# Optimization experiments

Measured on AMD Instinct MI355X. Metric: run time of the kernel, lower is better.

The kernel has to match this reference:

```python
import jax, jax.numpy as jnp
import numpy as np

G, M_PER_GROUP, K, N = 8, 2048, 4096, 4096  # experts, tokens/expert, d_model, expert out dim


def setup_inputs() -> dict:
    key = jax.random.key(0)
    k1, k2, k3, k4 = jax.random.split(key, 4)
    T = G * M_PER_GROUP
    # int8 quantized activations [total_tokens, K] and per-expert weights [G, N, K] ('NT' layout)
    i8_left_tensor = jax.random.randint(k1, (T, K), -127, 128, dtype=jnp.int32).astype(jnp.int8)
    i8_right_tensors = jax.random.randint(k2, (G, N, K), -127, 128, dtype=jnp.int32).astype(jnp.int8)
    # per-token and per-(group, out-channel) dequant scales
    left_scales = jax.random.uniform(k3, (T,), jnp.float32, 0.001, 0.02)
    right_scales = jax.random.uniform(k4, (G, N), jnp.float32, 0.001, 0.02)
    tokens_per_group = jnp.full((G,), M_PER_GROUP, dtype=jnp.int32)
    return {
        "i8_left_tensor": i8_left_tensor,
        "i8_right_tensors": i8_right_tensors,
        "left_scales": left_scales,
        "right_scales": right_scales,
        "tokens_per_group": tokens_per_group,
    }


def reference(i8_left_tensor, i8_right_tensors, left_scales, right_scales, tokens_per_group):
    # moe_w8a8_group_gemm, 'NT': per group g, out_g = (A_g @ B_g^T) * ls_g[:, None] * rs_g[None, :] -> fp16
    g, n, k = i8_right_tensors.shape
    t = i8_left_tensor.shape[0]
    m = t // g  # equal-sized groups (tokens_per_group is constant M_PER_GROUP)
    a = i8_left_tensor.reshape(g, m, k).astype(jnp.float32)   # [G, M, K]
    b = i8_right_tensors.astype(jnp.float32)                  # [G, N, K]
    acc = jnp.einsum('gmk,gnk->gmn', a, b)                    # int8xint8 accum in f32
    ls = left_scales.reshape(g, m, 1)
    rs = right_scales[:, None, :]
    out = (acc * ls * rs).astype(jnp.float16)                 # fused dequant epilogue
    return out.reshape(t, n)
```

## Files before the change

kernel.cpp:

```cpp
#include <hip/hip_runtime.h>

#define GG 8
#define MPG 2048
#define KD 4096
#define ND 4096

using i32x4 = __attribute__((ext_vector_type(4))) int;

__device__ __forceinline__ int pack4(i32x4 v) {
  return (int)((unsigned)(v[0] & 0xff) | ((unsigned)(v[1] & 0xff) << 8) |
               ((unsigned)(v[2] & 0xff) << 16) | ((unsigned)(v[3] & 0xff) << 24));
}

__global__ void conv_kernel(const int* __restrict__ src, char* __restrict__ dst, long nelem) {
  long t = (long)blockIdx.x * blockDim.x + threadIdx.x;
  long stride = (long)gridDim.x * blockDim.x;
  for (long e = t * 16; e < nelem; e += stride * 16) {
    i32x4 x0 = *(const i32x4*)(src + e);
    i32x4 x1 = *(const i32x4*)(src + e + 4);
    i32x4 x2 = *(const i32x4*)(src + e + 8);
    i32x4 x3 = *(const i32x4*)(src + e + 12);
    i32x4 p;
    p[0] = pack4(x0); p[1] = pack4(x1); p[2] = pack4(x2); p[3] = pack4(x3);
    *(i32x4*)(dst + e) = p;
  }
}

__device__ __forceinline__ void gload_lds16(const void* g, void* l) {
  __builtin_amdgcn_global_load_lds(
      (const __attribute__((address_space(1))) unsigned int*)g,
      (__attribute__((address_space(3))) unsigned int*)l, 16, 0, 0);
}

#define CFENCE() asm volatile("" ::: "memory")

constexpr int NT = KD / 128;

__global__ __launch_bounds__(512, 2) void gemm256_i8(
    const char* __restrict__ Aall,
    const char* __restrict__ Ball,
    const float* __restrict__ ls,
    const float* __restrict__ rs,
    float* __restrict__ out,
    int g0, int nwg)
{
  extern __shared__ char lds[];

  const int tid  = threadIdx.x;
  const int lane = tid & 63;
  const int wave = tid >> 6;

  int bid = blockIdx.x;
  int wg  = (bid & 7) * (nwg >> 3) + (bid >> 3);
  const int gl = wg >> 7;
  const int rr_ = wg & 127;
  const int bm = (rr_ >> 4) * 256;
  const int bn = (rr_ & 15) * 256;
  const int g  = g0 + gl;

  const int srow = tid >> 3;
  const int scol = ((tid & 7) << 4) ^ ((srow & 7) << 4);
  const char* Ag = Aall + ((size_t)gl * MPG + bm) * KD;
  const char* Bg = Ball + ((size_t)gl * ND  + bn) * KD;
  const char* pa[4]; const char* pb[4];
#pragma unroll
  for (int i = 0; i < 4; ++i) {
    pa[i] = Ag + (size_t)(i * 64 + srow) * KD + scol;
    pb[i] = Bg + (size_t)(i * 64 + srow) * KD + scol;
  }
  char* wbase = lds + wave * 1024;

  auto stageA = [&](int buf, int kt) {
    const int ko = kt << 7;
    char* d = wbase + buf * 65536;
#pragma unroll
    for (int i = 0; i < 4; ++i) gload_lds16(pa[i] + ko, d + i * 8192);
  };
  auto stageB = [&](int buf, int kt) {
    const int ko = kt << 7;
    char* d = wbase + buf * 65536 + 32768;
#pragma unroll
    for (int i = 0; i < 4; ++i) gload_lds16(pb[i] + ko, d + i * 8192);
  };

  const int wm = wave >> 2;
  const int wn = wave & 3;
  const int r16 = lane & 15;
  const int klane = (lane >> 4) << 4;
  const int sx = (r16 & 7) << 4;
  const char* aBase0 = lds + (size_t)(wm * 128 + r16) * 128;
  const char* bBase0 = lds + 32768 + (size_t)(wn * 64 + r16) * 128;

  i32x4 acc[8][4] = {};

  stageA(0, 0); stageB(0, 0);
  stageA(1, 1); stageB(1, 1);

#pragma unroll 1
  for (int kt = 0; kt < NT; ++kt) {
    const int c = kt & 1;
    const char* pA = aBase0 + c * 65536;
    const char* pB = bBase0 + c * 65536;
    const int kx0 = klane ^ sx;
    const int kx1 = (64 + klane) ^ sx;

    if (kt + 1 < NT) { asm volatile("s_waitcnt vmcnt(8)" ::: "memory"); }
    else             { asm volatile("s_waitcnt vmcnt(0)" ::: "memory"); }
    __builtin_amdgcn_s_barrier();
    CFENCE();

    i32x4 bf0[4], bf1[4], af0[4], af1[4];
#pragma unroll
    for (int n = 0; n < 4; ++n) bf0[n] = *(const i32x4*)(pB + n * 2048 + kx0);
#pragma unroll
    for (int m = 0; m < 4; ++m) af0[m] = *(const i32x4*)(pA + m * 2048 + kx0);
#pragma unroll
    for (int m = 0; m < 4; ++m) af1[m] = *(const i32x4*)(pA + (4 + m) * 2048 + kx0);
    __builtin_amdgcn_s_setprio(1);
#pragma unroll
    for (int m = 0; m < 4; ++m)
#pragma unroll
      for (int n = 0; n < 4; ++n)
        acc[m][n] = __builtin_amdgcn_mfma_i32_16x16x64_i8(af0[m], bf0[n], acc[m][n], 0, 0, 0);
    __builtin_amdgcn_s_setprio(0);
#pragma unroll
    for (int n = 0; n < 4; ++n) bf1[n] = *(const i32x4*)(pB + n * 2048 + kx1);
#pragma unroll
    for (int m = 0; m < 4; ++m) af0[m] = *(const i32x4*)(pA + m * 2048 + kx1);
    __builtin_amdgcn_s_setprio(1);
#pragma unroll
    for (int m = 0; m < 4; ++m)
#pragma unroll
      for (int n = 0; n < 4; ++n)
        acc[4 + m][n] = __builtin_amdgcn_mfma_i32_16x16x64_i8(af1[m], bf0[n], acc[4 + m][n], 0, 0, 0);
    __builtin_amdgcn_s_setprio(0);
#pragma unroll
    for (int m = 0; m < 4; ++m) af1[m] = *(const i32x4*)(pA + (4 + m) * 2048 + kx1);
    __builtin_amdgcn_s_setprio(1);
#pragma unroll
    for (int m = 0; m < 4; ++m)
#pragma unroll
      for (int n = 0; n < 4; ++n)
        acc[m][n] = __builtin_amdgcn_mfma_i32_16x16x64_i8(af0[m], bf1[n], acc[m][n], 0, 0, 0);
#pragma unroll
    for (int m = 0; m < 4; ++m)
#pragma unroll
      for (int n = 0; n < 4; ++n)
        acc[4 + m][n] = __builtin_amdgcn_mfma_i32_16x16x64_i8(af1[m], bf1[n], acc[4 + m][n], 0, 0, 0);
    __builtin_amdgcn_s_setprio(0);

    asm volatile("s_waitcnt lgkmcnt(0)" ::: "memory");
    __builtin_amdgcn_sched_barrier(0);
    __builtin_amdgcn_s_barrier();
    CFENCE();
    if (kt + 2 < NT) { stageA(c, kt + 2); stageB(c, kt + 2); }
  }

  const size_t orow0 = (size_t)g * MPG + bm + wm * 128 + ((lane >> 4) << 2);
  const int col0 = bn + wn * 64 + r16;
  float rsv[4];
#pragma unroll
  for (int n = 0; n < 4; ++n) rsv[n] = rs[(size_t)g * ND + col0 + n * 16];
#pragma unroll
  for (int m = 0; m < 8; ++m) {
#pragma unroll
    for (int q = 0; q < 4; ++q) {
      size_t row = orow0 + m * 16 + q;
      float lsv = ls[row];
#pragma unroll
      for (int n = 0; n < 4; ++n)
        out[row * ND + col0 + n * 16] = (float)acc[m][n][q] * lsv * rsv[n];
    }
  }
}

constexpr int BM = 128, BN = 128, BK = 64;

template<bool DIRECT>
__global__ __launch_bounds__(256) void gemm_i8(
    const void* __restrict__ Aptr, const void* __restrict__ Bptr,
    const float* __restrict__ ls, const float* __restrict__ rs,
    float* __restrict__ out, int g0)
{
  __shared__ char lA[BM * BK];
  __shared__ char lB[BN * BK];

  const int gl = blockIdx.z;
  const int g = g0 + gl;
  const int bm = blockIdx.y * BM;
  const int bn = blockIdx.x * BN;
  const int tid = threadIdx.x;
  const int lane = tid & 63;
  const int wave = tid >> 6;
  const int wr = (wave >> 1) * 64;
  const int wc = (wave & 1) * 64;
  const int r16 = lane & 15;
  const int kb = (lane >> 4) * 16;

  i32x4 acc[4][4] = {};

  if constexpr (!DIRECT) {
    const char* Ag = (const char*)Aptr + ((size_t)gl * MPG + bm) * KD;
    const char* Bg = (const char*)Bptr + ((size_t)gl * ND + bn) * KD;
    const int srow = tid >> 2;
    const int skoff = (tid & 3) * 16;
    const char* pa0 = Ag + (size_t)srow * KD + skoff;
    const char* pa1 = Ag + (size_t)(srow + 64) * KD + skoff;
    const char* pb0 = Bg + (size_t)srow * KD + skoff;
    const char* pb1 = Bg + (size_t)(srow + 64) * KD + skoff;
    char* la0 = lA + wave * 1024;
    char* la1 = lA + 4096 + wave * 1024;
    char* lb0 = lB + wave * 1024;
    char* lb1 = lB + 4096 + wave * 1024;

    for (int k0 = 0; k0 < KD; k0 += BK) {
      gload_lds16(pa0 + k0, la0);
      gload_lds16(pa1 + k0, la1);
      gload_lds16(pb0 + k0, lb0);
      gload_lds16(pb1 + k0, lb1);
      __syncthreads();
      i32x4 af[4], bf[4];
#pragma unroll
      for (int m = 0; m < 4; ++m) af[m] = *(const i32x4*)(lA + (wr + m * 16 + r16) * BK + kb);
#pragma unroll
      for (int n = 0; n < 4; ++n) bf[n] = *(const i32x4*)(lB + (wc + n * 16 + r16) * BK + kb);
#pragma unroll
      for (int m = 0; m < 4; ++m)
#pragma unroll
        for (int n = 0; n < 4; ++n)
          acc[m][n] = __builtin_amdgcn_mfma_i32_16x16x64_i8(af[m], bf[n], acc[m][n], 0, 0, 0);
      __syncthreads();
    }
  } else {
    const int* Ag = (const int*)Aptr + ((size_t)gl * MPG + bm) * KD;
    const int* Bg = (const int*)Bptr + ((size_t)gl * ND + bn) * KD;
    const int drow = tid >> 1;
    const int dk = (tid & 1) * 32;

    for (int k0 = 0; k0 < KD; k0 += BK) {
      int pa[8], pb[8];
#pragma unroll
      for (int j = 0; j < 8; ++j) pa[j] = pack4(*(const i32x4*)(Ag + (size_t)drow * KD + k0 + dk + j * 4));
#pragma unroll
      for (int j = 0; j < 8; ++j) pb[j] = pack4(*(const i32x4*)(Bg + (size_t)drow * KD + k0 + dk + j * 4));
      __syncthreads();
      *(i32x4*)(lA + drow * 64 + dk)      = *(i32x4*)(pa);
      *(i32x4*)(lA + drow * 64 + dk + 16) = *(i32x4*)(pa + 4);
      *(i32x4*)(lB + drow * 64 + dk)      = *(i32x4*)(pb);
      *(i32x4*)(lB + drow * 64 + dk + 16) = *(i32x4*)(pb + 4);
      __syncthreads();
      i32x4 af[4], bf[4];
#pragma unroll
      for (int m = 0; m < 4; ++m) af[m] = *(const i32x4*)(lA + (wr + m * 16 + r16) * BK + kb);
#pragma unroll
      for (int n = 0; n < 4; ++n) bf[n] = *(const i32x4*)(lB + (wc + n * 16 + r16) * BK + kb);
#pragma unroll
      for (int m = 0; m < 4; ++m)
#pragma unroll
        for (int n = 0; n < 4; ++n)
          acc[m][n] = __builtin_amdgcn_mfma_i32_16x16x64_i8(af[m], bf[n], acc[m][n], 0, 0, 0);
    }
  }

  const size_t trow0 = (size_t)g * MPG + bm + wr + (lane >> 4) * 4;
  const int col0 = bn + wc + r16;
  float rsv[4];
#pragma unroll
  for (int n = 0; n < 4; ++n) rsv[n] = rs[(size_t)g * ND + col0 + n * 16];
#pragma unroll
  for (int m = 0; m < 4; ++m) {
#pragma unroll
    for (int q = 0; q < 4; ++q) {
      size_t row = trow0 + m * 16 + q;
      float lsv = ls[row];
#pragma unroll
      for (int n = 0; n < 4; ++n)
        out[row * ND + col0 + n * 16] = (float)acc[m][n][q] * lsv * rsv[n];
    }
  }
}

extern "C" void kernel_launch(void* const* d_in, const int* in_sizes, int n_in,
                              void* d_out, int out_size, void* d_ws, size_t ws_size,
                              hipStream_t stream) {
  const int* A32 = (const int*)d_in[0];
  const int* B32 = (const int*)d_in[1];
  const float* ls = (const float*)d_in[2];
  const float* rs = (const float*)d_in[3];
  float* out = (float*)d_out;

  const size_t aE = (size_t)GG * MPG * KD;
  const size_t bE = (size_t)GG * ND * KD;
  const size_t aSlab = (size_t)MPG * KD;
  const size_t bSlab = (size_t)ND * KD;

  const int smem = 131072;
  bool big_lds_ok =
      hipFuncSetAttribute((const void*)gemm256_i8,
                          hipFuncAttributeMaxDynamicSharedMemorySize, smem) == hipSuccess;

  if (d_ws && ws_size >= aE + bE) {
    char* wsA = (char*)d_ws;
    char* wsB = wsA + aE;
    conv_kernel<<<8192, 256, 0, stream>>>(A32, wsA, (long)aE);
    conv_kernel<<<16384, 256, 0, stream>>>(B32, wsB, (long)bE);
    if (big_lds_ok) {
      gemm256_i8<<<1024, 512, smem, stream>>>(wsA, wsB, ls, rs, out, 0, 1024);
    } else {
      dim3 grid(ND / BN, MPG / BM, GG);
      gemm_i8<false><<<grid, dim3(256), 0, stream>>>(wsA, wsB, ls, rs, out, 0);
    }
  } else if (d_ws && ws_size >= aSlab + bSlab) {
    char* wsA = (char*)d_ws;
    char* wsB = wsA + aSlab;
    for (int gidx = 0; gidx < GG; ++gidx) {
      conv_kernel<<<2048, 256, 0, stream>>>(A32 + (size_t)gidx * aSlab, wsA, (long)aSlab);
      conv_kernel<<<4096, 256, 0, stream>>>(B32 + (size_t)gidx * bSlab, wsB, (long)bSlab);
      if (big_lds_ok) {
        gemm256_i8<<<128, 512, smem, stream>>>(wsA, wsB, ls, rs, out, gidx, 128);
      } else {
        dim3 grid(ND / BN, MPG / BM, 1);
        gemm_i8<false><<<grid, dim3(256), 0, stream>>>(wsA, wsB, ls, rs, out, gidx);
      }
    }
  } else {
    dim3 grid(ND / BN, MPG / BM, GG);
    gemm_i8<true><<<grid, dim3(256), 0, stream>>>(A32, B32, ls, rs, out, 0);
  }
}
```

Baseline: 496.6 us.

## Load B fragments directly from global into registers, keep only A in LDS

The B operand no longer goes through LDS. Each wave loads its B fragments straight from global memory into registers, while A keeps a double-buffered LDS path with one barrier per k-step. This halves dynamic LDS to 64 KB, removes the B staging and the second barrier per iteration, and may allow more workgroups per CU. In exchange, global-load latency for B sits directly in front of the MFMAs, the per-lane loads stride across rows and coalesce poorly, and waves that share columns fetch the same B data twice.

Measured after the change: 562.6 us. +13.3%, slower.

```diff
diff --git a/kernel.cpp b/kernel.cpp
--- a/kernel.cpp
+++ b/kernel.cpp
@@ -61,26 +61,16 @@
   const int srow = tid >> 3;
   const int scol = ((tid & 7) << 4) ^ ((srow & 7) << 4);
   const char* Ag = Aall + ((size_t)gl * MPG + bm) * KD;
-  const char* Bg = Ball + ((size_t)gl * ND  + bn) * KD;
-  const char* pa[4]; const char* pb[4];
-#pragma unroll
-  for (int i = 0; i < 4; ++i) {
-    pa[i] = Ag + (size_t)(i * 64 + srow) * KD + scol;
-    pb[i] = Bg + (size_t)(i * 64 + srow) * KD + scol;
-  }
+  const char* pa[4];
+#pragma unroll
+  for (int i = 0; i < 4; ++i) pa[i] = Ag + (size_t)(i * 64 + srow) * KD + scol;
   char* wbase = lds + wave * 1024;
 
   auto stageA = [&](int buf, int kt) {
     const int ko = kt << 7;
-    char* d = wbase + buf * 65536;
+    char* d = wbase + buf * 32768;
 #pragma unroll
     for (int i = 0; i < 4; ++i) gload_lds16(pa[i] + ko, d + i * 8192);
-  };
-  auto stageB = [&](int buf, int kt) {
-    const int ko = kt << 7;
-    char* d = wbase + buf * 65536 + 32768;
-#pragma unroll
-    for (int i = 0; i < 4; ++i) gload_lds16(pb[i] + ko, d + i * 8192);
   };
 
   const int wm = wave >> 2;
@@ -88,32 +78,42 @@
   const int r16 = lane & 15;
   const int klane = (lane >> 4) << 4;
   const int sx = (r16 & 7) << 4;
-  const char* aBase0 = lds + (size_t)(wm * 128 + r16) * 128;
-  const char* bBase0 = lds + 32768 + (size_t)(wn * 64 + r16) * 128;
+  const int aoff = (wm * 128 + r16) * 128;
+  const int kx0 = klane ^ sx;
+  const int kx1 = (64 + klane) ^ sx;
+  const char* Blane = Ball + ((size_t)gl * ND + bn + wn * 64 + r16) * KD;
 
   i32x4 acc[8][4] = {};
 
-  stageA(0, 0); stageB(0, 0);
-  stageA(1, 1); stageB(1, 1);
+  stageA(0, 0);
 
 #pragma unroll 1
   for (int kt = 0; kt < NT; ++kt) {
     const int c = kt & 1;
-    const char* pA = aBase0 + c * 65536;
-    const char* pB = bBase0 + c * 65536;
-    const int kx0 = klane ^ sx;
-    const int kx1 = (64 + klane) ^ sx;
-
-    if (kt + 1 < NT) { asm volatile("s_waitcnt vmcnt(8)" ::: "memory"); }
-    else             { asm volatile("s_waitcnt vmcnt(0)" ::: "memory"); }
+    const char* pA = lds + c * 32768 + aoff;
+    const int ko = kt << 7;
+    i32x4 bf[4], af0[4], af1[4];
+
+#pragma unroll
+    for (int n = 0; n < 4; ++n)
+      bf[n] = *(const i32x4*)(Blane + (size_t)(n * 16) * KD + ko + klane);
+    CFENCE();
+    asm volatile("s_waitcnt vmcnt(4)" ::: "memory");
     __builtin_amdgcn_s_barrier();
     CFENCE();
-
-    i32x4 bf0[4], bf1[4], af0[4], af1[4];
-#pragma unroll
-    for (int n = 0; n < 4; ++n) bf0[n] = *(const i32x4*)(pB + n * 2048 + kx0);
+    if (kt + 1 < NT) stageA(c ^ 1, kt + 1);
+    __builtin_amdgcn_sched_barrier(0);
+
 #pragma unroll
     for (int m = 0; m < 4; ++m) af0[m] = *(const i32x4*)(pA + m * 2048 + kx0);
+    __builtin_amdgcn_s_setprio(1);
+#pragma unroll
+    for (int m = 0; m < 4; ++m)
+#pragma unroll
+      for (int n = 0; n < 4; ++n)
+        acc[m][n] = __builtin_amdgcn_mfma_i32_16x16x64_i8(af0[m], bf[n], acc[m][n], 0, 0, 0);
+    __builtin_amdgcn_s_setprio(0);
+
 #pragma unroll
     for (int m = 0; m < 4; ++m) af1[m] = *(const i32x4*)(pA + (4 + m) * 2048 + kx0);
     __builtin_amdgcn_s_setprio(1);
@@ -121,10 +121,13 @@
     for (int m = 0; m < 4; ++m)
 #pragma unroll
       for (int n = 0; n < 4; ++n)
-        acc[m][n] = __builtin_amdgcn_mfma_i32_16x16x64_i8(af0[m], bf0[n], acc[m][n], 0, 0, 0);
+        acc[4 + m][n] = __builtin_amdgcn_mfma_i32_16x16x64_i8(af1[m], bf[n], acc[4 + m][n], 0, 0, 0);
     __builtin_amdgcn_s_setprio(0);
-#pragma unroll
-    for (int n = 0; n < 4; ++n) bf1[n] = *(const i32x4*)(pB + n * 2048 + kx1);
+
+#pragma unroll
+    for (int n = 0; n < 4; ++n)
+      bf[n] = *(const i32x4*)(Blane + (size_t)(n * 16) * KD + ko + 64 + klane);
+
 #pragma unroll
     for (int m = 0; m < 4; ++m) af0[m] = *(const i32x4*)(pA + m * 2048 + kx1);
     __builtin_amdgcn_s_setprio(1);
@@ -132,8 +135,9 @@
     for (int m = 0; m < 4; ++m)
 #pragma unroll
       for (int n = 0; n < 4; ++n)
-        acc[4 + m][n] = __builtin_amdgcn_mfma_i32_16x16x64_i8(af1[m], bf0[n], acc[4 + m][n], 0, 0, 0);
+        acc[m][n] = __builtin_amdgcn_mfma_i32_16x16x64_i8(af0[m], bf[n], acc[m][n], 0, 0, 0);
     __builtin_amdgcn_s_setprio(0);
+
 #pragma unroll
     for (int m = 0; m < 4; ++m) af1[m] = *(const i32x4*)(pA + (4 + m) * 2048 + kx1);
     __builtin_amdgcn_s_setprio(1);
@@ -141,19 +145,8 @@
     for (int m = 0; m < 4; ++m)
 #pragma unroll
       for (int n = 0; n < 4; ++n)
-        acc[m][n] = __builtin_amdgcn_mfma_i32_16x16x64_i8(af0[m], bf1[n], acc[m][n], 0, 0, 0);
-#pragma unroll
-    for (int m = 0; m < 4; ++m)
-#pragma unroll
-      for (int n = 0; n < 4; ++n)
-        acc[4 + m][n] = __builtin_amdgcn_mfma_i32_16x16x64_i8(af1[m], bf1[n], acc[4 + m][n], 0, 0, 0);
+        acc[4 + m][n] = __builtin_amdgcn_mfma_i32_16x16x64_i8(af1[m], bf[n], acc[4 + m][n], 0, 0, 0);
     __builtin_amdgcn_s_setprio(0);
-
-    asm volatile("s_waitcnt lgkmcnt(0)" ::: "memory");
-    __builtin_amdgcn_sched_barrier(0);
-    __builtin_amdgcn_s_barrier();
-    CFENCE();
-    if (kt + 2 < NT) { stageA(c, kt + 2); stageB(c, kt + 2); }
   }
 
   const size_t orow0 = (size_t)g * MPG + bm + wm * 128 + ((lane >> 4) << 2);
@@ -294,7 +287,7 @@
   const size_t aSlab = (size_t)MPG * KD;
   const size_t bSlab = (size_t)ND * KD;
 
-  const int smem = 131072;
+  const int smem = 65536;
   bool big_lds_ok =
       hipFuncSetAttribute((const void*)gemm256_i8,
                           hipFuncAttributeMaxDynamicSharedMemorySize, smem) == hipSuccess;
```
